# Kernel optimization log

Hardware: AMD Instinct MI355X
Metric: run time of the kernel (lower is better)

The kernel has to match this reference:

```python
import jax, jax.numpy as jnp
import numpy as np

B, S, D, H = 2, 1024, 1024, 8
HD = D // H            # head_dim = 128
NBUCKETS = 64          # bucket_size (number of hash buckets)
NEG = -1e30


def setup_inputs() -> dict:
    key = jax.random.key(0)
    ks = jax.random.split(key, 10)
    scale = D ** -0.5
    return {
        "x": jax.random.normal(ks[0], (B, S, D), dtype=jnp.float32),
        "Wq": jax.random.normal(ks[1], (D, D), dtype=jnp.float32) * scale,
        "bq": jnp.zeros((D,), dtype=jnp.float32),
        "Wk": jax.random.normal(ks[2], (D, D), dtype=jnp.float32) * scale,
        "bk": jnp.zeros((D,), dtype=jnp.float32),
        "Wv": jax.random.normal(ks[3], (D, D), dtype=jnp.float32) * scale,
        "bv": jnp.zeros((D,), dtype=jnp.float32),
        "Wo": jax.random.normal(ks[4], (D, D), dtype=jnp.float32) * scale,
        "bo": jnp.zeros((D,), dtype=jnp.float32),
        "hash_proj": jax.random.normal(ks[5], (H, HD, NBUCKETS), dtype=jnp.float32),
    }


def reference(x, Wq, bq, Wk, bk, Wv, bv, Wo, bo, hash_proj):
    b, s, d = x.shape
    n = b * s  # buckets gather (batch, token) pairs jointly -> flatten batch into tokens

    def split_heads(y):  # [B,S,D] -> [H, B*S, HD]
        return y.reshape(b, s, H, HD).transpose(2, 0, 1, 3).reshape(H, n, HD)

    q = split_heads(x @ Wq + bq)
    k = split_heads(x @ Wk + bk)
    v = split_heads(x @ Wv + bv)

    # learned LSH routing: argmax over hash projections per head
    hash_scores = jnp.einsum('hnd,hdf->hnf', q, hash_proj)
    buckets = jnp.argmax(hash_scores, axis=-1)  # [H, N] int

    # per-bucket attention == masked dense attention with same-bucket mask
    dots = jnp.einsum('hnd,hmd->hnm', q, k) / (HD ** 0.5)  # [H,N,N]
    same = buckets[:, :, None] == buckets[:, None, :]
    attn = jax.nn.softmax(jnp.where(same, dots, NEG), axis=-1)
    o = jnp.einsum('hnm,hmd->hnd', attn, v)  # [H,N,HD]

    out = o.reshape(H, b, s, HD).transpose(1, 2, 0, 3).reshape(b, s, d)
    return out @ Wo + bo
```

## Files before the change

kernel.cpp:

```cpp
#include <hip/hip_runtime.h>
#include <stdint.h>

typedef __attribute__((ext_vector_type(8))) short short8;
typedef __attribute__((ext_vector_type(4))) short short4v;
typedef __attribute__((ext_vector_type(4))) float float4v;
typedef unsigned short u16;

#define N_TOK 2048
#define D_MODEL 1024
#define N_HEAD 8
#define HDIM 128
#define N_BUCKET 64
#define WL_CAP 2048
#define ATTN_BLOCKS 384

__device__ __forceinline__ u16 f2bf(float f) {
  uint32_t u = __float_as_uint(f);
  uint32_t r = u + 0x7fffu + ((u >> 16) & 1u);
  return (u16)(r >> 16);
}
__device__ __forceinline__ float bf2f(u16 h) {
  return __uint_as_float(((uint32_t)h) << 16);
}

__device__ __forceinline__ void async_load16(const void* g, void* l) {
  __builtin_amdgcn_global_load_lds(
      (const __attribute__((address_space(1))) void*)g,
      (__attribute__((address_space(3))) void*)l, 16, 0, 0);
}

__device__ __forceinline__ int xcd_swz(int bid, int nwg) {
  return (bid & 7) * (nwg >> 3) + (bid >> 3);
}

__global__ __launch_bounds__(256) void prep_kernel(
    const float* __restrict__ x, const float* __restrict__ Wq,
    const float* __restrict__ Wk, const float* __restrict__ Wv,
    const float* __restrict__ Wo, const float* __restrict__ proj,
    u16* __restrict__ xhi, u16* __restrict__ xlo,
    u16* __restrict__ wqt_hi, u16* __restrict__ wqt_lo, u16* __restrict__ kvt,
    u16* __restrict__ wot, u16* __restrict__ projt_hi,
    u16* __restrict__ projt_lo, int* __restrict__ counts) {
  const int z = blockIdx.z;
  if (z == 4) {
    int base = (blockIdx.y * 32 + blockIdx.x) * 2048 + threadIdx.x * 8;
    float4v a = *(const float4v*)&x[base];
    float4v b = *(const float4v*)&x[base + 4];
    short8 hi, lo;
#pragma unroll
    for (int j = 0; j < 4; j++) {
      u16 h = f2bf(a[j]);
      hi[j] = (short)h;
      lo[j] = (short)f2bf(a[j] - bf2f(h));
    }
#pragma unroll
    for (int j = 0; j < 4; j++) {
      u16 h = f2bf(b[j]);
      hi[4 + j] = (short)h;
      lo[4 + j] = (short)f2bf(b[j] - bf2f(h));
    }
    *(short8*)&xhi[base] = hi;
    *(short8*)&xlo[base] = lo;
    return;
  }
  __shared__ float tile[32][33];
  int tx = threadIdx.x & 31, ty = threadIdx.x >> 5;
  if (z == 5) {
    if (blockIdx.x == 2) {
      if (blockIdx.y == 0) {
        counts[threadIdx.x] = 0;
        counts[threadIdx.x + 256] = 0;
      }
      return;
    }
    if (blockIdx.x > 2) return;
    const int head = blockIdx.y >> 2;
    const int r0 = (blockIdx.y & 3) * 32;
    const int c0 = blockIdx.x * 32;
    const float* in = proj + (size_t)head * 128 * 64;
#pragma unroll
    for (int i = 0; i < 4; i++) {
      int rl = ty + i * 8;
      tile[rl][tx] = in[(size_t)(r0 + rl) * 64 + c0 + tx];
    }
    __syncthreads();
#pragma unroll
    for (int i = 0; i < 4; i++) {
      int cl = ty + i * 8;
      float v = tile[tx][cl];
      size_t oidx = (size_t)head * 64 * 128 + (size_t)(c0 + cl) * 128 + r0 + tx;
      u16 h = f2bf(v);
      projt_hi[oidx] = h;
      projt_lo[oidx] = f2bf(v - bf2f(h));
    }
    return;
  }
  const float* in = (z == 0) ? Wq : (z == 1) ? Wk : (z == 2) ? Wv : Wo;
  u16* hi = (z == 0) ? wqt_hi
            : (z == 1) ? kvt
            : (z == 2) ? (kvt + (size_t)1024 * 1024) : wot;
  u16* lo = (z == 0) ? wqt_lo : nullptr;
  const int C = 1024, R = 1024;
  int c0 = blockIdx.x * 32, r0 = blockIdx.y * 32;
#pragma unroll
  for (int i = 0; i < 4; i++) {
    int rl = ty + i * 8;
    tile[rl][tx] = in[(size_t)(r0 + rl) * C + c0 + tx];
  }
  __syncthreads();
#pragma unroll
  for (int i = 0; i < 4; i++) {
    int cl = ty + i * 8;
    float v = tile[tx][cl];
    size_t oidx = (size_t)(c0 + cl) * R + r0 + tx;
    u16 h = f2bf(v);
    hi[oidx] = h;
    if (lo) lo[oidx] = f2bf(v - bf2f(h));
  }
}

template <int BM>
__device__ __forceinline__ void stage_tiles2(const u16* A, const u16* Bt,
                                             u16* As, u16* Bs, int bm, int bn,
                                             int K, int ko, int wave, int lane) {
  const int arow = lane >> 2;
  const int acolb = (lane & 3) * 16;
  constexpr int ACH = BM / 16;
  constexpr int PC = (ACH + 8) / 4;
#pragma unroll
  for (int cc = 0; cc < PC; cc++) {
    int idx = wave * PC + cc;
    if (idx < ACH) {
      int row = idx * 16 + arow;
      const char* g = (const char*)A + ((size_t)(bm + row) * K + ko) * 2 + acolb;
      async_load16(g, (char*)As + idx * 1024);
    } else {
      int row = (idx - ACH) * 16 + arow;
      const char* g = (const char*)Bt + ((size_t)(bn + row) * K + ko) * 2 + acolb;
      async_load16(g, (char*)Bs + (idx - ACH) * 1024);
    }
  }
}

template <int BM>
__global__ __launch_bounds__(256) void gemm_bf16_kernel(
    const u16* __restrict__ A, const u16* __restrict__ Bt,
    float* __restrict__ C, const float* __restrict__ bias,
    const float* __restrict__ bias2, u16* __restrict__ kbf,
    u16* __restrict__ vbf, int N, int K, int flags) {
  constexpr int MI = BM / 32;
  __shared__ __align__(16) u16 As[2][BM * 32];
  __shared__ __align__(16) u16 Bs[2][128 * 32];
  const int tid = threadIdx.x;
  const int wave = tid >> 6, lane = tid & 63;
  const int lhi = lane >> 4, llo = lane & 15;
  const int nbn = N >> 7;
  const int bid = xcd_swz(blockIdx.x, gridDim.x);
  const int bm = (bid / nbn) * BM;
  const int bn = (bid % nbn) << 7;
  const int wm = (BM == 128) ? (wave >> 1) * 64 : (wave & 1) * 32;
  const int wn = (BM == 128) ? (wave & 1) * 64 : (wave >> 1) * 64;

  float4v acc[MI][4];
#pragma unroll
  for (int mi = 0; mi < MI; mi++)
#pragma unroll
    for (int ni = 0; ni < 4; ni++)
#pragma unroll
      for (int r = 0; r < 4; r++) acc[mi][ni][r] = 0.f;

  stage_tiles2<BM>(A, Bt, As[0], Bs[0], bm, bn, K, 0, wave, lane);
  __syncthreads();
  const int nk = K >> 5;
  for (int t = 0; t < nk; t++) {
    const int cur = t & 1;
    if (t + 1 < nk)
      stage_tiles2<BM>(A, Bt, As[cur ^ 1], Bs[cur ^ 1], bm, bn, K,
                       (t + 1) << 5, wave, lane);
    short8 af[MI], bfr[4];
#pragma unroll
    for (int i = 0; i < MI; i++)
      af[i] = *(const short8*)&As[cur][(wm + i * 16 + llo) * 32 + lhi * 8];
#pragma unroll
    for (int i = 0; i < 4; i++)
      bfr[i] = *(const short8*)&Bs[cur][(wn + i * 16 + llo) * 32 + lhi * 8];
#pragma unroll
    for (int mi = 0; mi < MI; mi++)
#pragma unroll
      for (int ni = 0; ni < 4; ni++)
        acc[mi][ni] = __builtin_amdgcn_mfma_f32_16x16x32_bf16(af[mi], bfr[ni],
                                                              acc[mi][ni], 0, 0, 0);
    __syncthreads();
  }

#pragma unroll
  for (int mi = 0; mi < MI; mi++)
#pragma unroll
    for (int ni = 0; ni < 4; ni++) {
      int row0 = bm + wm + mi * 16 + lhi * 4;
      int col = bn + wn + ni * 16 + llo;
      if (flags & 8) {
        u16* dst = (col < 1024) ? kbf : vbf;
        int c = col & 1023;
        float bb = (col < 1024) ? bias[c] : bias2[c];
#pragma unroll
        for (int r = 0; r < 4; r++)
          dst[(size_t)(row0 + r) * 1024 + c] = f2bf(acc[mi][ni][r] + bb);
      } else {
        float bb = (flags & 2) ? bias[col] : 0.f;
        float* cp = C + (size_t)row0 * N + col;
#pragma unroll
        for (int r = 0; r < 4; r++) cp[(size_t)r * N] = acc[mi][ni][r] + bb;
      }
    }
}

#define QROW 136
__global__ __launch_bounds__(256) void proj_gemm_kernel(
    const u16* __restrict__ A0, const u16* __restrict__ A1,
    const u16* __restrict__ B0, const u16* __restrict__ B1,
    const u16* __restrict__ kvt, const u16* __restrict__ projt_hi,
    const u16* __restrict__ projt_lo, const float* __restrict__ bq,
    const float* __restrict__ bk, const float* __restrict__ bv,
    u16* __restrict__ qbb, int* __restrict__ bucket,
    u16* __restrict__ kbf, u16* __restrict__ vbf, int* __restrict__ counts) {
  __shared__ __align__(16) u16 S3[2][12288];
  const int tid = threadIdx.x;
  const int wave = tid >> 6, lane = tid & 63;
  const int lhi = lane >> 4, llo = lane & 15;
  const int arow = lane >> 2;
  const int acolb = (lane & 3) * 16;
  const int K = 1024;
  const int b = blockIdx.x;
  const int cls = b % 3;

  if (cls == 0) {
    const int bid = b / 3;
    const int bm = (bid >> 3) * 64;
    const int bn = (bid & 7) << 7;
    const int wm = (wave & 1) * 32;
    const int wn = (wave >> 1) * 64;

    float4v acc[2][4];
#pragma unroll
    for (int mi = 0; mi < 2; mi++)
#pragma unroll
      for (int ni = 0; ni < 4; ni++)
#pragma unroll
        for (int r = 0; r < 4; r++) acc[mi][ni][r] = 0.f;

    auto stage = [&](int bb2, int ko) {
      char* base = (char*)&S3[bb2][0];
#pragma unroll
      for (int cc = 0; cc < 6; cc++) {
        int idx = wave * 6 + cc;
        const u16* src;
        int row;
        char* dst;
        if (idx < 4) {
          src = A0; row = bm + idx * 16 + arow; dst = base + idx * 1024;
        } else if (idx < 8) {
          src = A1; row = bm + (idx - 4) * 16 + arow; dst = base + 4096 + (idx - 4) * 1024;
        } else if (idx < 16) {
          src = B0; row = bn + (idx - 8) * 16 + arow; dst = base + 8192 + (idx - 8) * 1024;
        } else {
          src = B1; row = bn + (idx - 16) * 16 + arow; dst = base + 16384 + (idx - 16) * 1024;
        }
        async_load16((const char*)src + ((size_t)row * K + ko) * 2 + acolb, dst);
      }
    };

    stage(0, 0);
    __syncthreads();
    for (int t = 0; t < 32; t++) {
      const int cur = t & 1;
      if (t + 1 < 32) stage(cur ^ 1, (t + 1) << 5);
      const u16* Sc = &S3[cur][0];
      short8 afh[2], afl[2], bfh[4], bfl[4];
#pragma unroll
      for (int i = 0; i < 2; i++) {
        afh[i] = *(const short8*)&Sc[(wm + i * 16 + llo) * 32 + lhi * 8];
        afl[i] = *(const short8*)&Sc[2048 + (wm + i * 16 + llo) * 32 + lhi * 8];
      }
#pragma unroll
      for (int i = 0; i < 4; i++) {
        bfh[i] = *(const short8*)&Sc[4096 + (wn + i * 16 + llo) * 32 + lhi * 8];
        bfl[i] = *(const short8*)&Sc[8192 + (wn + i * 16 + llo) * 32 + lhi * 8];
      }
#pragma unroll
      for (int mi = 0; mi < 2; mi++)
#pragma unroll
        for (int ni = 0; ni < 4; ni++)
          acc[mi][ni] = __builtin_amdgcn_mfma_f32_16x16x32_bf16(afh[mi], bfh[ni],
                                                                acc[mi][ni], 0, 0, 0);
#pragma unroll
      for (int mi = 0; mi < 2; mi++)
#pragma unroll
        for (int ni = 0; ni < 4; ni++)
          acc[mi][ni] = __builtin_amdgcn_mfma_f32_16x16x32_bf16(afh[mi], bfl[ni],
                                                                acc[mi][ni], 0, 0, 0);
#pragma unroll
      for (int mi = 0; mi < 2; mi++)
#pragma unroll
        for (int ni = 0; ni < 4; ni++)
          acc[mi][ni] = __builtin_amdgcn_mfma_f32_16x16x32_bf16(afl[mi], bfh[ni],
                                                                acc[mi][ni], 0, 0, 0);
      __syncthreads();
    }

    u16* sQh = &S3[0][0];
    u16* sQl = &S3[0][64 * QROW];
#pragma unroll
    for (int mi = 0; mi < 2; mi++)
#pragma unroll
      for (int ni = 0; ni < 4; ni++) {
        int rl0 = wm + mi * 16 + lhi * 4;
        int col = wn + ni * 16 + llo;
        float bb = bq[bn + col];
#pragma unroll
        for (int r = 0; r < 4; r++) {
          float v = acc[mi][ni][r] + bb;
          u16 h = f2bf(v);
          qbb[(size_t)(bm + rl0 + r) * 1024 + bn + col] = h;
          sQh[(rl0 + r) * QROW + col] = h;
          sQl[(rl0 + r) * QROW + col] = f2bf(v - bf2f(h));
        }
      }
    __syncthreads();

    {
      const int h = bn >> 7;
      const int wm2 = wave * 16;
      short8 qh[4], ql[4];
#pragma unroll
      for (int kf = 0; kf < 4; kf++) {
        qh[kf] = *(const short8*)&sQh[(wm2 + llo) * QROW + kf * 32 + lhi * 8];
        ql[kf] = *(const short8*)&sQl[(wm2 + llo) * QROW + kf * 32 + lhi * 8];
      }
      const u16* ph = projt_hi + (size_t)h * 64 * 128;
      const u16* pl = projt_lo + (size_t)h * 64 * 128;
      float4v sc2[4];
#pragma unroll
      for (int nf = 0; nf < 4; nf++)
#pragma unroll
        for (int r = 0; r < 4; r++) sc2[nf][r] = 0.f;
#pragma unroll
      for (int nf = 0; nf < 4; nf++) {
        int brow = (nf * 16 + llo) * 128;
#pragma unroll
        for (int kf = 0; kf < 4; kf++) {
          short8 bh = *(const short8*)&ph[brow + kf * 32 + lhi * 8];
          short8 bl = *(const short8*)&pl[brow + kf * 32 + lhi * 8];
          sc2[nf] = __builtin_amdgcn_mfma_f32_16x16x32_bf16(qh[kf], bh, sc2[nf], 0, 0, 0);
          sc2[nf] = __builtin_amdgcn_mfma_f32_16x16x32_bf16(qh[kf], bl, sc2[nf], 0, 0, 0);
          sc2[nf] = __builtin_amdgcn_mfma_f32_16x16x32_bf16(ql[kf], bh, sc2[nf], 0, 0, 0);
        }
      }
#pragma unroll
      for (int r = 0; r < 4; r++) {
        float best = sc2[0][r];
        int bi = llo;
#pragma unroll
        for (int nf = 1; nf < 4; nf++) {
          float v = sc2[nf][r];
          if (v > best) { best = v; bi = nf * 16 + llo; }
        }
#pragma unroll
        for (int o = 1; o < 16; o <<= 1) {
          float ov = __shfl_xor(best, o);
          int oi = __shfl_xor(bi, o);
          if (ov > best || (ov == best && oi < bi)) { best = ov; bi = oi; }
        }
        if (llo == 0) {
          bucket[h * N_TOK + bm + wm2 + lhi * 4 + r] = bi;
          atomicAdd(&counts[h * 64 + bi], 1);
        }
      }
    }
  } else {
    const int bid2 = (b / 3) * 2 + (cls - 1);
    const int bm = (bid2 >> 4) * 64;
    const int bn = (bid2 & 15) << 7;
    const int wm = (wave & 1) * 32;
    const int wn = (wave >> 1) * 64;

    float4v acc[2][4];
#pragma unroll
    for (int mi = 0; mi < 2; mi++)
#pragma unroll
      for (int ni = 0; ni < 4; ni++)
#pragma unroll
        for (int r = 0; r < 4; r++) acc[mi][ni][r] = 0.f;

    stage_tiles2<64>(A0, kvt, &S3[0][0], &S3[0][4096], bm, bn, K, 0, wave, lane);
    __syncthreads();
    for (int t = 0; t < 32; t++) {
      const int cur = t & 1;
      if (t + 1 < 32)
        stage_tiles2<64>(A0, kvt, &S3[0][(cur ^ 1) * 2048],
                         &S3[0][4096 + (cur ^ 1) * 4096], bm, bn, K,
                         (t + 1) << 5, wave, lane);
      const u16* Ac = &S3[0][cur * 2048];
      const u16* Bc = &S3[0][4096 + cur * 4096];
      short8 af[2], bfr[4];
#pragma unroll
      for (int i = 0; i < 2; i++)
        af[i] = *(const short8*)&Ac[(wm + i * 16 + llo) * 32 + lhi * 8];
#pragma unroll
      for (int i = 0; i < 4; i++)
        bfr[i] = *(const short8*)&Bc[(wn + i * 16 + llo) * 32 + lhi * 8];
#pragma unroll
      for (int mi = 0; mi < 2; mi++)
#pragma unroll
        for (int ni = 0; ni < 4; ni++)
          acc[mi][ni] = __builtin_amdgcn_mfma_f32_16x16x32_bf16(af[mi], bfr[ni],
                                                                acc[mi][ni], 0, 0, 0);
      __syncthreads();
    }

#pragma unroll
    for (int mi = 0; mi < 2; mi++)
#pragma unroll
      for (int ni = 0; ni < 4; ni++) {
        int row0 = bm + wm + mi * 16 + lhi * 4;
        int col = bn + wn + ni * 16 + llo;
        u16* dst = (col < 1024) ? kbf : vbf;
        int c = col & 1023;
        float bb = (col < 1024) ? bk[c] : bv[c];
#pragma unroll
        for (int r = 0; r < 4; r++)
          dst[(size_t)(row0 + r) * 1024 + c] = f2bf(acc[mi][ni][r] + bb);
      }
  }
}

__global__ __launch_bounds__(64) void fillwl_kernel(
    const int* __restrict__ bucket, const int* __restrict__ counts,
    int* __restrict__ offsets_g, int* __restrict__ perm,
    int* __restrict__ wl, int* __restrict__ wl_count) {
  const int hb = blockIdx.x;
  const int h = hb >> 6, b = hb & 63;
  const int lane = threadIdx.x;
  int offp = 0, wlp = 0;
#pragma unroll
  for (int i = 0; i < 8; i++) {
    int idx = i * 64 + lane;
    int c = counts[idx];
    int nq = (c + 15) >> 4;
    if (idx < hb) { offp += c; wlp += nq; }
  }
#pragma unroll
  for (int o = 1; o < 64; o <<= 1) {
    offp += __shfl_xor(offp, o);
    wlp += __shfl_xor(wlp, o);
  }
  const int cnt = counts[hb];
  const int nq = (cnt + 15) >> 4;
  if (lane == 0) offsets_g[hb] = offp;
  for (int i = lane; i < nq; i += 64) wl[wlp + i] = (h << 13) | (b << 7) | i;
  if (hb == 511 && lane == 0) wl_count[0] = wlp + nq;
  int base = offp;
  for (int t = 0; t < N_TOK; t += 64) {
    int tok = t + lane;
    bool match = bucket[h * N_TOK + tok] == b;
    unsigned long long mask = __ballot(match);
    if (match) {
      int pos = base + __popcll(mask & ((1ull << lane) - 1ull));
      perm[pos] = tok;
    }
    base += __popcll(mask);
  }
}

__global__ __launch_bounds__(256) void gather_vt_kernel(
    const u16* __restrict__ vbb, const int* __restrict__ perm,
    u16* __restrict__ Vts) {
  __shared__ u16 lds[64][72];
  int bid = blockIdx.x;
  int h = bid >> 6;
  int ptile = (bid & 63) >> 1;
  int d0 = (bid & 1) * 64;
  int pos0 = ptile * 64;
  int t = threadIdx.x;
#pragma unroll
  for (int i = 0; i < 2; i++) {
    int unit = t + 256 * i;
    int p = unit >> 3, seg = unit & 7;
    int tok = perm[h * N_TOK + pos0 + p];
    short8 v = *(const short8*)&vbb[(size_t)tok * D_MODEL + h * HDIM + d0 + seg * 8];
    *(short8*)&lds[p][seg * 8] = v;
  }
  __syncthreads();
#pragma unroll
  for (int i = 0; i < 8; i++) {
    int unit = t + 256 * i;
    int drow = unit >> 5, pp = unit & 31;
    uint32_t val = (uint32_t)lds[2 * pp][drow] |
                   ((uint32_t)lds[2 * pp + 1][drow] << 16);
    uint32_t* dst = (uint32_t*)&Vts[(size_t)(h * HDIM + d0 + drow) * N_TOK + pos0];
    dst[pp] = val;
  }
}

__global__ __launch_bounds__(256) void attn_bucket_kernel(
    const u16* __restrict__ qbb, const u16* __restrict__ kbb,
    const u16* __restrict__ Vts, const int* __restrict__ perm,
    const int* __restrict__ offsets, const int* __restrict__ counts,
    const int* __restrict__ wl, const int* __restrict__ wl_count,
    u16* __restrict__ ob) {
  const int wave = threadIdx.x >> 6, lane = threadIdx.x & 63;
  const int lhi = lane >> 4, llo = lane & 15;
  const int wslot = blockIdx.x * 4 + wave;
  const int NW = ATTN_BLOCKS * 4;
  const int cnt = wl_count[0];
  __shared__ __align__(16) u16 P_lds[4][16][64];
  const float scale = 0.08838834764831845f;

  for (int e = wslot; e < cnt; e += NW) {
    int ent = wl[e];
    int h = ent >> 13, qt = ent & 127;
    int hb = (h << 6) | ((ent >> 7) & 63);
    int off = offsets[hb];
    int bs = counts[hb];
    int offh = off - h * N_TOK;
    int qbase = qt * 16;

    int qr = qbase + llo;
    int tokq = perm[off + min(qr, bs - 1)];
    const u16* qrow = &qbb[(size_t)tokq * D_MODEL + h * HDIM];
    short8 qf[4];
#pragma unroll
    for (int kf = 0; kf < 4; kf++)
      qf[kf] = *(const short8*)&qrow[kf * 32 + lhi * 8];

    float m[4], l[4];
#pragma unroll
    for (int r = 0; r < 4; r++) { m[r] = -INFINITY; l[r] = 0.f; }
    float4v accO[8];
#pragma unroll
    for (int d = 0; d < 8; d++)
#pragma unroll
      for (int r = 0; r < 4; r++) accO[d][r] = 0.f;

    for (int c0 = 0; c0 < bs; c0 += 64) {
      float4v scv[4];
#pragma unroll
      for (int nf = 0; nf < 4; nf++)
#pragma unroll
        for (int r = 0; r < 4; r++) scv[nf][r] = 0.f;
#pragma unroll
      for (int nf = 0; nf < 4; nf++) {
        int kcol = c0 + nf * 16 + llo;
        int tokk = perm[off + min(kcol, bs - 1)];
        const u16* krow = &kbb[(size_t)tokk * D_MODEL + h * HDIM];
#pragma unroll
        for (int kf = 0; kf < 4; kf++) {
          short8 kfr = *(const short8*)&krow[kf * 32 + lhi * 8];
          scv[nf] = __builtin_amdgcn_mfma_f32_16x16x32_bf16(qf[kf], kfr, scv[nf], 0, 0, 0);
        }
      }

      float tmax[4];
#pragma unroll
      for (int r = 0; r < 4; r++) tmax[r] = -INFINITY;
#pragma unroll
      for (int nf = 0; nf < 4; nf++) {
        bool valid = (c0 + nf * 16 + llo) < bs;
#pragma unroll
        for (int r = 0; r < 4; r++) {
          float v = valid ? scv[nf][r] * scale : -1e30f;
          scv[nf][r] = v;
          tmax[r] = fmaxf(tmax[r], v);
        }
      }
#pragma unroll
      for (int r = 0; r < 4; r++)
#pragma unroll
        for (int o = 1; o < 16; o <<= 1)
          tmax[r] = fmaxf(tmax[r], __shfl_xor(tmax[r], o));

      float resc[4], psum[4];
#pragma unroll
      for (int r = 0; r < 4; r++) {
        float mn = fmaxf(m[r], tmax[r]);
        resc[r] = __expf(m[r] - mn);
        m[r] = mn;
        psum[r] = 0.f;
      }
#pragma unroll
      for (int nf = 0; nf < 4; nf++)
#pragma unroll
        for (int r = 0; r < 4; r++) {
          float p = __expf(scv[nf][r] - m[r]);
          psum[r] += p;
          P_lds[wave][lhi * 4 + r][nf * 16 + llo] = f2bf(p);
        }
#pragma unroll
      for (int r = 0; r < 4; r++) {
#pragma unroll
        for (int o = 1; o < 16; o <<= 1) psum[r] += __shfl_xor(psum[r], o);
        l[r] = l[r] * resc[r] + psum[r];
      }
#pragma unroll
      for (int d = 0; d < 8; d++)
#pragma unroll
        for (int r = 0; r < 4; r++) accO[d][r] *= resc[r];

      asm volatile("s_waitcnt lgkmcnt(0)" ::: "memory");
      short8 pf[2];
#pragma unroll
      for (int k2 = 0; k2 < 2; k2++)
        pf[k2] = *(const short8*)&P_lds[wave][llo][k2 * 32 + lhi * 8];
#pragma unroll
      for (int d = 0; d < 8; d++)
#pragma unroll
        for (int k2 = 0; k2 < 2; k2++) {
          short8 vfr = *(const short8*)&Vts[(size_t)(h * HDIM + d * 16 + llo) * N_TOK +
                                            offh + c0 + k2 * 32 + lhi * 8];
          accO[d] = __builtin_amdgcn_mfma_f32_16x16x32_bf16(pf[k2], vfr, accO[d], 0, 0, 0);
        }
      asm volatile("" ::: "memory");
    }

#pragma unroll
    for (int r = 0; r < 4; r++) {
      int rl = qbase + lhi * 4 + r;
      if (rl < bs) {
        int tok = perm[off + rl];
        float inv = 1.f / l[r];
#pragma unroll
        for (int d = 0; d < 8; d++)
          ob[(size_t)tok * D_MODEL + h * HDIM + d * 16 + llo] = f2bf(accO[d][r] * inv);
      }
    }
  }
}

extern "C" void kernel_launch(void* const* d_in, const int* in_sizes, int n_in,
                              void* d_out, int out_size, void* d_ws, size_t ws_size,
                              hipStream_t stream) {
  const float* x  = (const float*)d_in[0];
  const float* Wq = (const float*)d_in[1];
  const float* bq = (const float*)d_in[2];
  const float* Wk = (const float*)d_in[3];
  const float* bk = (const float*)d_in[4];
  const float* Wv = (const float*)d_in[5];
  const float* bv = (const float*)d_in[6];
  const float* Wo = (const float*)d_in[7];
  const float* bo = (const float*)d_in[8];
  const float* hp = (const float*)d_in[9];
  float* out = (float*)d_out;

  char* ws = (char*)d_ws;
  size_t off = 0;
  auto alloc = [&](size_t b) {
    char* p = ws + off;
    off += (b + 255) & ~(size_t)255;
    return p;
  };

  const int N = N_TOK, D = D_MODEL;
  u16* xhi    = (u16*)alloc((size_t)N * D * 2);
  u16* xlo    = (u16*)alloc((size_t)N * D * 2);
  u16* wqt_hi = (u16*)alloc((size_t)D * D * 2);
  u16* wqt_lo = (u16*)alloc((size_t)D * D * 2);
  u16* kvt    = (u16*)alloc((size_t)2 * D * D * 2);
  u16* wot    = (u16*)alloc((size_t)D * D * 2);
  u16* pjt_hi = (u16*)alloc((size_t)N_HEAD * 64 * 128 * 2);
  u16* pjt_lo = (u16*)alloc((size_t)N_HEAD * 64 * 128 * 2);
  u16* qbb    = (u16*)alloc((size_t)N * D * 2);
  u16* kbb    = (u16*)alloc((size_t)N * D * 2);
  u16* vbb    = (u16*)alloc((size_t)N * D * 2);
  u16* Vts    = (u16*)alloc((size_t)N_HEAD * HDIM * N * 2 + 256);
  int* bucket = (int*)alloc((size_t)N_HEAD * N * 4);
  int* counts = (int*)alloc(512 * 4);
  int* offs   = (int*)alloc(512 * 4);
  int* perm   = (int*)alloc((size_t)N_HEAD * N * 4);
  int* wl     = (int*)alloc(WL_CAP * 4);
  int* wlcnt  = (int*)alloc(256);
  u16* ob     = (u16*)alloc((size_t)N * D * 2);

  prep_kernel<<<dim3(32, 32, 6), 256, 0, stream>>>(
      x, Wq, Wk, Wv, Wo, hp, xhi, xlo, wqt_hi, wqt_lo, kvt, wot, pjt_hi,
      pjt_lo, counts);

  proj_gemm_kernel<<<768, 256, 0, stream>>>(
      xhi, xlo, wqt_hi, wqt_lo, kvt, pjt_hi, pjt_lo, bq, bk, bv,
      qbb, bucket, kbb, vbb, counts);

  fillwl_kernel<<<512, 64, 0, stream>>>(bucket, counts, offs, perm, wl, wlcnt);
  gather_vt_kernel<<<512, 256, 0, stream>>>(vbb, perm, Vts);

  attn_bucket_kernel<<<ATTN_BLOCKS, 256, 0, stream>>>(
      qbb, kbb, Vts, perm, offs, counts, wl, wlcnt, ob);

  gemm_bf16_kernel<64><<<(N / 64) * (D / 128), 256, 0, stream>>>(
      ob, wot, out, bo, nullptr, nullptr, nullptr, D, D, 2);

  (void)in_sizes; (void)n_in; (void)out_size; (void)ws_size;
}
```

Before: 114.2 us.

## Compute bucket counts in fillwl and deepen K/V GEMM K-tile with swizzled LDS

Drops the per-token atomic histogram from the projection GEMM. Each fillwl block now counts its own bucket and the tokens in lower buckets by ballot over the bucket array, and claims work-list slots with one atomic. The K/V projection path switches to 64-wide K tiles staged through direct global-to-LDS loads with an XOR swizzle, halving the loop iterations and barriers. The cost is that every fillwl block rescans all tokens of its head, and the work-list order now depends on atomic timing, so it is no longer deterministic.

```diff
diff --git a/kernel.cpp b/kernel.cpp
--- a/kernel.cpp
+++ b/kernel.cpp
@@ -40,7 +40,7 @@
     u16* __restrict__ xhi, u16* __restrict__ xlo,
     u16* __restrict__ wqt_hi, u16* __restrict__ wqt_lo, u16* __restrict__ kvt,
     u16* __restrict__ wot, u16* __restrict__ projt_hi,
-    u16* __restrict__ projt_lo, int* __restrict__ counts) {
+    u16* __restrict__ projt_lo, int* __restrict__ wlcnt) {
   const int z = blockIdx.z;
   if (z == 4) {
     int base = (blockIdx.y * 32 + blockIdx.x) * 2048 + threadIdx.x * 8;
@@ -67,10 +67,7 @@
   int tx = threadIdx.x & 31, ty = threadIdx.x >> 5;
   if (z == 5) {
     if (blockIdx.x == 2) {
-      if (blockIdx.y == 0) {
-        counts[threadIdx.x] = 0;
-        counts[threadIdx.x + 256] = 0;
-      }
+      if (blockIdx.y == 0 && threadIdx.x == 0) wlcnt[0] = 0;
       return;
     }
     if (blockIdx.x > 2) return;
@@ -223,7 +220,7 @@
     const u16* __restrict__ projt_lo, const float* __restrict__ bq,
     const float* __restrict__ bk, const float* __restrict__ bv,
     u16* __restrict__ qbb, int* __restrict__ bucket,
-    u16* __restrict__ kbf, u16* __restrict__ vbf, int* __restrict__ counts) {
+    u16* __restrict__ kbf, u16* __restrict__ vbf) {
   __shared__ __align__(16) u16 S3[2][12288];
   const int tid = threadIdx.x;
   const int wave = tid >> 6, lane = tid & 63;
@@ -371,10 +368,7 @@
           int oi = __shfl_xor(bi, o);
           if (ov > best || (ov == best && oi < bi)) { best = ov; bi = oi; }
         }
-        if (llo == 0) {
-          bucket[h * N_TOK + bm + wm2 + lhi * 4 + r] = bi;
-          atomicAdd(&counts[h * 64 + bi], 1);
-        }
+        if (llo == 0) bucket[h * N_TOK + bm + wm2 + lhi * 4 + r] = bi;
       }
     }
   } else {
@@ -383,6 +377,7 @@
     const int bn = (bid2 & 15) << 7;
     const int wm = (wave & 1) * 32;
     const int wn = (wave >> 1) * 64;
+    const int swz = (llo & 7) << 3;
 
     float4v acc[2][4];
 #pragma unroll
@@ -392,29 +387,57 @@
 #pragma unroll
         for (int r = 0; r < 4; r++) acc[mi][ni][r] = 0.f;
 
-    stage_tiles2<64>(A0, kvt, &S3[0][0], &S3[0][4096], bm, bn, K, 0, wave, lane);
+    const int crow = lane >> 3;
+    const int ccolb = (((lane & 7) ^ (lane >> 3)) << 4);
+
+    auto stageKV = [&](int bb2, int ko) {
+#pragma unroll
+      for (int cc = 0; cc < 6; cc++) {
+        int idx = wave * 6 + cc;
+        const u16* src;
+        int grow;
+        u16* dstb;
+        if (idx < 8) {
+          src = A0;
+          grow = bm + idx * 8 + crow;
+          dstb = &S3[0][bb2 * 4096 + idx * 512];
+        } else {
+          src = kvt;
+          grow = bn + (idx - 8) * 8 + crow;
+          dstb = &S3[0][8192 + bb2 * 8192 + (idx - 8) * 512];
+        }
+        async_load16((const char*)src + ((size_t)grow * K + ko) * 2 + ccolb, dstb);
+      }
+    };
+
+    stageKV(0, 0);
     __syncthreads();
-    for (int t = 0; t < 32; t++) {
+    for (int t = 0; t < 16; t++) {
       const int cur = t & 1;
-      if (t + 1 < 32)
-        stage_tiles2<64>(A0, kvt, &S3[0][(cur ^ 1) * 2048],
-                         &S3[0][4096 + (cur ^ 1) * 4096], bm, bn, K,
-                         (t + 1) << 5, wave, lane);
-      const u16* Ac = &S3[0][cur * 2048];
-      const u16* Bc = &S3[0][4096 + cur * 4096];
-      short8 af[2], bfr[4];
-#pragma unroll
-      for (int i = 0; i < 2; i++)
-        af[i] = *(const short8*)&Ac[(wm + i * 16 + llo) * 32 + lhi * 8];
-#pragma unroll
-      for (int i = 0; i < 4; i++)
-        bfr[i] = *(const short8*)&Bc[(wn + i * 16 + llo) * 32 + lhi * 8];
+      if (t + 1 < 16) stageKV(cur ^ 1, (t + 1) << 6);
+      const u16* Ac = &S3[0][cur * 4096];
+      const u16* Bc = &S3[0][8192 + cur * 8192];
+      short8 af[2][2], bfr[4][2];
 #pragma unroll
       for (int mi = 0; mi < 2; mi++)
 #pragma unroll
-        for (int ni = 0; ni < 4; ni++)
-          acc[mi][ni] = __builtin_amdgcn_mfma_f32_16x16x32_bf16(af[mi], bfr[ni],
-                                                                acc[mi][ni], 0, 0, 0);
+        for (int kk = 0; kk < 2; kk++)
+          af[mi][kk] = *(const short8*)&Ac[(wm + mi * 16 + llo) * 64 +
+                                           ((kk * 32 + lhi * 8) ^ swz)];
+#pragma unroll
+      for (int ni = 0; ni < 4; ni++)
+#pragma unroll
+        for (int kk = 0; kk < 2; kk++)
+          bfr[ni][kk] = *(const short8*)&Bc[(wn + ni * 16 + llo) * 64 +
+                                            ((kk * 32 + lhi * 8) ^ swz)];
+#pragma unroll
+      for (int kk = 0; kk < 2; kk++)
+#pragma unroll
+        for (int mi = 0; mi < 2; mi++)
+#pragma unroll
+          for (int ni = 0; ni < 4; ni++)
+            acc[mi][ni] = __builtin_amdgcn_mfma_f32_16x16x32_bf16(
+                af[mi][kk], bfr[ni][kk], acc[mi][ni], 0, 0, 0);
       __syncthreads();
     }
 
@@ -435,30 +458,28 @@
 }
 
 __global__ __launch_bounds__(64) void fillwl_kernel(
-    const int* __restrict__ bucket, const int* __restrict__ counts,
+    const int* __restrict__ bucket, int* __restrict__ counts_g,
     int* __restrict__ offsets_g, int* __restrict__ perm,
     int* __restrict__ wl, int* __restrict__ wl_count) {
   const int hb = blockIdx.x;
   const int h = hb >> 6, b = hb & 63;
   const int lane = threadIdx.x;
-  int offp = 0, wlp = 0;
-#pragma unroll
-  for (int i = 0; i < 8; i++) {
-    int idx = i * 64 + lane;
-    int c = counts[idx];
-    int nq = (c + 15) >> 4;
-    if (idx < hb) { offp += c; wlp += nq; }
-  }
-#pragma unroll
-  for (int o = 1; o < 64; o <<= 1) {
-    offp += __shfl_xor(offp, o);
-    wlp += __shfl_xor(wlp, o);
-  }
-  const int cnt = counts[hb];
+  int cnt = 0, cnt_lt = 0;
+  for (int t = 0; t < N_TOK; t += 64) {
+    int bt = bucket[h * N_TOK + t + lane];
+    cnt += __popcll(__ballot(bt == b));
+    cnt_lt += __popcll(__ballot(bt < b));
+  }
+  const int offp = h * N_TOK + cnt_lt;
   const int nq = (cnt + 15) >> 4;
-  if (lane == 0) offsets_g[hb] = offp;
-  for (int i = lane; i < nq; i += 64) wl[wlp + i] = (h << 13) | (b << 7) | i;
-  if (hb == 511 && lane == 0) wl_count[0] = wlp + nq;
+  if (lane == 0) {
+    counts_g[hb] = cnt;
+    offsets_g[hb] = offp;
+  }
+  int sb = 0;
+  if (lane == 0) sb = atomicAdd(wl_count, nq);
+  sb = __shfl(sb, 0);
+  for (int i = lane; i < nq; i += 64) wl[sb + i] = (h << 13) | (b << 7) | i;
   int base = offp;
   for (int t = 0; t < N_TOK; t += 64) {
     int tok = t + lane;
@@ -682,11 +703,11 @@
 
   prep_kernel<<<dim3(32, 32, 6), 256, 0, stream>>>(
       x, Wq, Wk, Wv, Wo, hp, xhi, xlo, wqt_hi, wqt_lo, kvt, wot, pjt_hi,
-      pjt_lo, counts);
+      pjt_lo, wlcnt);
 
   proj_gemm_kernel<<<768, 256, 0, stream>>>(
       xhi, xlo, wqt_hi, wqt_lo, kvt, pjt_hi, pjt_lo, bq, bk, bv,
-      qbb, bucket, kbb, vbb, counts);
+      qbb, bucket, kbb, vbb);
 
   fillwl_kernel<<<512, 64, 0, stream>>>(bucket, counts, offs, perm, wl, wlcnt);
   gather_vt_kernel<<<512, 256, 0, stream>>>(vbb, perm, Vts);
```

Result: faster. 108.5 us (-5.0%).
